# Kernel tuning notes

Measured on AMD Instinct MI355X. Metric: run time of the kernel, lower is better.

## Reference

```python
import jax, jax.numpy as jnp
import numpy as np

N_USER = 60000
N_ITEM = 40000
N = N_USER + N_ITEM          # 100000 nodes
D = 64                       # embed / layer dim
NNZ = 1600000                # edges per relation (avg degree 16)
B = 16384                    # batch of (user,item) pairs
NLAYERS = 2                  # layers=[64,64,64] -> 2 GNN layers
VAL_SCALE = 0.02             # ~1/degree, mimics symmetric-normalized Laplacian values
W_SCALE = 0.05


def spmm(row, col, val, X):
    # sparse [N,N] @ dense [N,D] via gather + segment-sum (COO)
    return jax.ops.segment_sum(val[:, None] * X[col], row, num_segments=N)


def setup_inputs() -> dict:
    key = jax.random.key(0)
    ks = jax.random.split(key, 40)
    inp = {}
    inp['userIdx'] = jax.random.randint(ks[0], (B,), 0, N_USER, dtype=jnp.int32)
    inp['itemIdx'] = jax.random.randint(ks[1], (B,), 0, N_ITEM, dtype=jnp.int32)
    inp['uEmbd'] = jax.random.normal(ks[2], (N_USER, D), dtype=jnp.float32)
    inp['iEmbd'] = jax.random.normal(ks[3], (N_ITEM, D), dtype=jnp.float32)
    for i, name in enumerate(['lap', 'trust', 'add']):
        inp[name + '_row'] = jax.random.randint(ks[4 + 3 * i], (NNZ,), 0, N, dtype=jnp.int32)
        inp[name + '_col'] = jax.random.randint(ks[5 + 3 * i], (NNZ,), 0, N, dtype=jnp.int32)
        inp[name + '_val'] = jax.random.uniform(ks[6 + 3 * i], (NNZ,), dtype=jnp.float32) * VAL_SCALE
    j = 13
    for name in ['lin_W', 'inter_W', 'attM_W', 'attA_W', 'attT_W']:
        inp[name] = jax.random.normal(ks[j], (NLAYERS, D, D), dtype=jnp.float32) * W_SCALE; j += 1
    for name in ['lin_b', 'inter_b', 'attM_b', 'attA_b', 'attT_b']:
        inp[name] = jax.random.normal(ks[j], (NLAYERS, D), dtype=jnp.float32) * W_SCALE; j += 1
    for name in ['a_main', 'a_add', 'a_trust']:
        inp[name] = jax.random.normal(ks[j], (NLAYERS, D, 1), dtype=jnp.float32) * W_SCALE; j += 1
    inp['W1'] = jax.random.normal(ks[j], (2 * D, 64), dtype=jnp.float32) * W_SCALE; j += 1
    inp['b1'] = jax.random.normal(ks[j], (64,), dtype=jnp.float32) * W_SCALE; j += 1
    inp['W2'] = jax.random.normal(ks[j], (64, 32), dtype=jnp.float32) * W_SCALE; j += 1
    inp['b2'] = jax.random.normal(ks[j], (32,), dtype=jnp.float32) * W_SCALE; j += 1
    inp['W3'] = jax.random.normal(ks[j], (32, 1), dtype=jnp.float32) * W_SCALE; j += 1
    inp['b3'] = jax.random.normal(ks[j], (1,), dtype=jnp.float32) * W_SCALE; j += 1
    return inp


def _gcf_forward(userIdx, itemIdx, uEmbd, iEmbd,
                 lap_row, lap_col, lap_val,
                 trust_row, trust_col, trust_val,
                 add_row, add_col, add_val,
                 lin_W, lin_b, inter_W, inter_b,
                 attM_W, attM_b, attA_W, attA_b, attT_W, attT_b,
                 a_main, a_add, a_trust,
                 W1, b1, W2, b2, W3, b3):
    feats = jnp.concatenate([uEmbd, iEmbd], axis=0)  # [N, D]
    all_emb = [feats]
    rels = [(lap_row, lap_col, lap_val),
            (trust_row, trust_col, trust_val),
            (add_row, add_col, add_val)]
    for l in range(NLAYERS):
        X = feats
        X2 = X * X  # inter_feature = features * features

        def relation(edges, aW, ab, avec):
            row, col, val = edges
            # (L + I) @ X  -> linear ; L @ (X*X) -> interActTransform
            h1 = (spmm(row, col, val, X) + X) @ lin_W[l] + lin_b[l]
            h2 = spmm(row, col, val, X2) @ inter_W[l] + inter_b[l]
            att = jnp.tanh((h1 + h2) @ aW + ab) @ avec  # [N, 1]
            return h1, h2, att.mean()

        m1, m2, w_main = relation(rels[0], attM_W[l], attM_b[l], a_main[l])
        t1, t2, w_trust = relation(rels[1], attT_W[l], attT_b[l], a_trust[l])
        a1, a2, w_add = relation(rels[2], attA_W[l], attA_b[l], a_add[l])
        beta = jax.nn.softmax(jnp.stack([w_main, w_add, w_trust]))  # [3]
        feats = (beta[0] * (m1 + m2) + beta[1] * (a1 + a2) + beta[2] * (t1 + t2))
        all_emb.append(feats)
    final = jnp.mean(jnp.stack(all_emb, axis=1), axis=1)  # [N, D]
    userE = final[userIdx]
    itemE = final[itemIdx + N_USER]
    h = jnp.concatenate([userE, itemE], axis=1)  # [B, 2D]
    h = jax.nn.relu(h @ W1 + b1)
    h = h @ W2 + b2
    h = h @ W3 + b3
    prediction = h.reshape(-1)
    return prediction, userE, itemE, final


def reference(userIdx, itemIdx, uEmbd, iEmbd,
              lap_row, lap_col, lap_val,
              trust_row, trust_col, trust_val,
              add_row, add_col, add_val,
              lin_W, lin_b, inter_W, inter_b,
              attM_W, attM_b, attA_W, attA_b, attT_W, attT_b,
              a_main, a_add, a_trust,
              W1, b1, W2, b2, W3, b3):
    return _gcf_forward(userIdx, itemIdx, uEmbd, iEmbd,
                        lap_row, lap_col, lap_val,
                        trust_row, trust_col, trust_val,
                        add_row, add_col, add_val,
                        lin_W, lin_b, inter_W, inter_b,
                        attM_W, attM_b, attA_W, attA_b, attT_W, attT_b,
                        a_main, a_add, a_trust,
                        W1, b1, W2, b2, W3, b3)
```

## Files before the change

### kernel.cpp

```cpp
#include <hip/hip_runtime.h>

#define N_USER  60000
#define N_ITEM  40000
#define NN      100000
#define NNZ_E   1600000
#define BB      16384
#define ND      6400000
#define ND4     1600000
#define NCHUNK  6250
#define NBUCK   196
#define BUCK_CAP 9216
#define BUCKTOT (NBUCK * BUCK_CAP)
#define BINB    196
#define EPB     8192

typedef __attribute__((ext_vector_type(8))) short bf16x8;
typedef __attribute__((ext_vector_type(8))) unsigned short u16x8;
typedef __attribute__((ext_vector_type(4))) float f32x4;

__device__ __forceinline__ float tanh_fast(float x) {
    x = fminf(fmaxf(x, -15.f), 15.f);
    float e = __expf(2.f * x);
    return (e - 1.f) / (e + 1.f);
}

__device__ __forceinline__ float bcast(float x, int k) {
    return __int_as_float(__builtin_amdgcn_readlane(__float_as_int(x), k));
}

__device__ __forceinline__ unsigned short f2bf(float f) {
    unsigned u = __float_as_uint(f);
    u += 0x7FFFu + ((u >> 16) & 1u);
    return (unsigned short)(u >> 16);
}
__device__ __forceinline__ float bf2f(unsigned short s) {
    return __uint_as_float(((unsigned)s) << 16);
}

__device__ __forceinline__ int widx(int k, int n) {
    return ((((n >> 4) * 2 + (k >> 5)) * 4 + ((k >> 3) & 3)) * 16 + (n & 15)) * 8 + (k & 7);
}

__global__ __launch_bounds__(256) void init_kernel(
    const float4* __restrict__ u, const float4* __restrict__ it,
    ushort* __restrict__ XB, float4* __restrict__ fs,
    int* __restrict__ CURS, float* __restrict__ attsum)
{
    int i = blockIdx.x * 256 + threadIdx.x;
    if (i < ND4) {
        float4 v = (i < N_USER * 16) ? u[i] : it[i - N_USER * 16];
        fs[i] = v;
        ushort4 b;
        b.x = f2bf(v.x); b.y = f2bf(v.y); b.z = f2bf(v.z); b.w = f2bf(v.w);
        ((ushort4*)XB)[i] = b;
    }
    if (i < 3 * NBUCK) CURS[i] = (i % NBUCK) * BUCK_CAP;
    if (i < 6) attsum[i] = 0.f;
}

__global__ __launch_bounds__(512) void bin_kernel(
    const int* __restrict__ rows0, const int* __restrict__ cols0, const float* __restrict__ vals0,
    const int* __restrict__ rows1, const int* __restrict__ cols1, const float* __restrict__ vals1,
    const int* __restrict__ rows2, const int* __restrict__ cols2, const float* __restrict__ vals2,
    int* __restrict__ CURS, int2* __restrict__ ECV)
{
    int rel = blockIdx.x / BINB;
    int blk = blockIdx.x % BINB;
    const int* rows; const int* cols; const float* vals;
    if (rel == 0) { rows = rows0; cols = cols0; vals = vals0; }
    else if (rel == 1) { rows = rows1; cols = cols1; vals = vals1; }
    else { rows = rows2; cols = cols2; vals = vals2; }
    long long* out = (long long*)(ECV + (size_t)rel * BUCKTOT);

    __shared__ int2 sStage[EPB];
    __shared__ int hW[8 * NBUCK];
    __shared__ int lOff[NBUCK], lEnd[NBUCK], lCur[NBUCK], gB[NBUCK];
    __shared__ int wt[4];

    int t = threadIdx.x;
    int lane = t & 63, w = t >> 6;
    for (int i = t; i < 8 * NBUCK; i += 512) hW[i] = 0;
    __syncthreads();

    int base = blk * EPB;
    int myrow[16];
    #pragma unroll
    for (int j = 0; j < 16; ++j) {
        int idx = base + j * 512 + t;
        myrow[j] = (idx < NNZ_E) ? __builtin_nontemporal_load(&rows[idx]) : -1;
        if (myrow[j] >= 0) atomicAdd(&hW[w * NBUCK + (myrow[j] >> 9)], 1);
    }
    __syncthreads();
    if (t < 256) {
        int h = 0;
        if (t < NBUCK) {
            #pragma unroll
            for (int ww = 0; ww < 8; ++ww) h += hW[ww * NBUCK + t];
        }
        int sc = h;
        #pragma unroll
        for (int o = 1; o < 64; o <<= 1) {
            int u = __shfl_up(sc, o);
            if (lane >= o) sc += u;
        }
        if (lane == 63) wt[w] = sc;
        __syncthreads();
        int woff = 0;
        #pragma unroll
        for (int ww = 0; ww < 4; ++ww) if (ww < w) woff += wt[ww];
        int excl = woff + sc - h;
        if (t < NBUCK) {
            lOff[t] = excl;
            lEnd[t] = excl + h;
            lCur[t] = excl;
            gB[t] = h ? atomicAdd(&CURS[rel * NBUCK + t], h) : 0;
        }
    } else {
        __syncthreads();
    }
    __syncthreads();
    #pragma unroll
    for (int j = 0; j < 16; ++j) {
        int idx = base + j * 512 + t;
        if (myrow[j] >= 0) {
            int c = __builtin_nontemporal_load(&cols[idx]);
            float v = __builtin_nontemporal_load(&vals[idx]);
            int b = myrow[j] >> 9;
            int pos = atomicAdd(&lCur[b], 1);
            int2 e;
            e.x = ((myrow[j] & 511) << 17) | c;
            e.y = __float_as_int(v);
            sStage[pos] = e;
        }
    }
    __syncthreads();
    for (int b = w; b < NBUCK; b += 8) {
        int s = lOff[b], e = lEnd[b];
        int gb = gB[b];
        int lim = (b + 1) * BUCK_CAP;
        for (int i = s + lane; i < e; i += 64) {
            int d = gb + (i - s);
            if (d < lim) {
                int2 ev = sStage[i];
                long long packed = (((long long)(unsigned)ev.y) << 32) | (unsigned)ev.x;
                __builtin_nontemporal_store(packed, &out[d]);
            }
        }
    }
}

__global__ __launch_bounds__(512) void bsort_kernel(
    const int* __restrict__ CURS, int2* __restrict__ ECV,
    int* __restrict__ RPS, int* __restrict__ RPE)
{
    int rel = blockIdx.x / NBUCK;
    int b   = blockIdx.x % NBUCK;
    int start = b * BUCK_CAP;
    int cnt = CURS[rel * NBUCK + b] - start;
    if (cnt > BUCK_CAP) cnt = BUCK_CAP;
    int2* ecv = ECV + (size_t)rel * BUCKTOT;

    __shared__ int2 sStage[BUCK_CAP];
    __shared__ int sOff[512], sCnt[512];
    __shared__ int wt[8];
    int t = threadIdx.x;
    int lane = t & 63, w = t >> 6;
    sCnt[t] = 0;
    __syncthreads();
    int2 e[18];
    #pragma unroll
    for (int j = 0; j < 18; ++j) {
        int i = t + j * 512;
        if (i < cnt) {
            e[j] = ecv[start + i];
            atomicAdd(&sCnt[((unsigned)e[j].x) >> 17], 1);
        }
    }
    __syncthreads();
    int h = sCnt[t];
    int sc = h;
    #pragma unroll
    for (int o = 1; o < 64; o <<= 1) {
        int u = __shfl_up(sc, o);
        if (lane >= o) sc += u;
    }
    if (lane == 63) wt[w] = sc;
    __syncthreads();
    int woff = 0;
    #pragma unroll
    for (int ww = 0; ww < 8; ++ww) if (ww < w) woff += wt[ww];
    int excl = woff + sc - h;
    __syncthreads();
    sOff[t] = excl;
    sCnt[t] = excl;
    __syncthreads();
    #pragma unroll
    for (int j = 0; j < 18; ++j) {
        int i = t + j * 512;
        if (i < cnt) {
            int rl = ((unsigned)e[j].x) >> 17;
            int pos = atomicAdd(&sCnt[rl], 1);
            int2 o2; o2.x = e[j].x & 0x1FFFF; o2.y = e[j].y;
            sStage[pos] = o2;
        }
    }
    __syncthreads();
    for (int i = t; i < cnt; i += 512) ecv[start + i] = sStage[i];
    int row = b * 512 + t;
    if (row < NN) {
        RPS[rel * NN + row] = start + sOff[t];
        RPE[rel * NN + row] = start + sCnt[t];
    }
}

__global__ __launch_bounds__(256, 4) void spmm_kernel(
    const int* __restrict__ RPS, const int* __restrict__ RPE,
    const int2* __restrict__ ecv,
    const ushort* __restrict__ XB, ushort* __restrict__ G)
{
    int t = threadIdx.x;
    int lane = t & 63;
    int wv = t >> 6;
    int dl = lane & 7;
    int r = blockIdx.x * 32 + wv * 8 + (lane >> 3);
    int ea = RPS[r], eb = RPE[r];
    int cnt = eb - ea;
    int cm = cnt;
    cm = max(cm, __shfl_xor(cm, 8));
    cm = max(cm, __shfl_xor(cm, 16));
    cm = max(cm, __shfl_xor(cm, 32));
    u16x8 xo8 = *(const u16x8*)&XB[(size_t)r * 64 + 8 * dl];
    float s1[8] = {0.f, 0.f, 0.f, 0.f, 0.f, 0.f, 0.f, 0.f};
    float s2[8] = {0.f, 0.f, 0.f, 0.f, 0.f, 0.f, 0.f, 0.f};
    for (int base = 0; base < cm; base += 4) {
        float vv[4]; u16x8 xx[4];
        #pragma unroll
        for (int j = 0; j < 4; ++j) {
            int i = base + j;
            bool ok = i < cnt;
            int is = ea + (ok ? i : 0);
            int2 cv = ecv[is];
            vv[j] = ok ? __int_as_float(cv.y) : 0.f;
            xx[j] = *(const u16x8*)&XB[(size_t)cv.x * 64 + 8 * dl];
        }
        #pragma unroll
        for (int j = 0; j < 4; ++j) {
            float v = vv[j];
            #pragma unroll
            for (int d = 0; d < 8; ++d) {
                float x = bf2f(xx[j][d]);
                s1[d] += v * x;
                s2[d] += v * x * x;
            }
        }
    }
    u16x8 o1, o2;
    #pragma unroll
    for (int d = 0; d < 8; ++d) {
        o1[d] = f2bf(s1[d] + bf2f(xo8[d]));
        o2[d] = f2bf(s2[d]);
    }
    *(u16x8*)&G[(size_t)r * 128 + 8 * dl]      = o1;
    *(u16x8*)&G[(size_t)r * 128 + 64 + 8 * dl] = o2;
}

__global__ __launch_bounds__(256) void dense_kernel(
    const ushort* __restrict__ G, ushort* __restrict__ Hout,
    const float* __restrict__ linW, const float* __restrict__ interW,
    const float* __restrict__ linb, const float* __restrict__ interb,
    const float* __restrict__ attW, const float* __restrict__ attb,
    const float* __restrict__ avec, float* __restrict__ attsum)
{
    __shared__ short sL[4096], sI[4096], sW[4096];
    __shared__ float sH[4 * 16 * 65];
    __shared__ float sBias[64], sAttb[64], sAvec[64];

    int tid = threadIdx.x;
    for (int i = tid; i < 4096; i += 256) {
        int k = i >> 6, n = i & 63, ix = widx(k, n);
        sL[ix] = (short)f2bf(linW[i]);
        sI[ix] = (short)f2bf(interW[i]);
        sW[ix] = (short)f2bf(attW[i]);
    }
    if (tid < 64) {
        sBias[tid] = linb[tid] + interb[tid];
        sAttb[tid] = attb[tid];
        sAvec[tid] = avec[tid];
    }
    __syncthreads();

    const bf16x8* pL = (const bf16x8*)sL;
    const bf16x8* pI = (const bf16x8*)sI;
    const bf16x8* pW = (const bf16x8*)sW;

    int lane = tid & 63;
    int wv = tid >> 6;
    int nl = lane & 15;
    int q  = lane >> 4;
    float* myH = sH + wv * (16 * 65);
    int gw = blockIdx.x * 4 + wv;
    int nw = gridDim.x * 4;
    float att_acc = 0.f;

    for (int c = gw; c < NCHUNK; c += nw) {
        int r0 = c * 16;
        const bf16x8* gp = (const bf16x8*)(G + (size_t)(r0 + nl) * 128);
        bf16x8 Ah[2], Qh[2];
        Ah[0] = gp[q];         Ah[1] = gp[4 + q];
        Qh[0] = gp[8 + q];     Qh[1] = gp[12 + q];
        #pragma unroll
        for (int nt = 0; nt < 4; ++nt) {
            float b = sBias[nt * 16 + nl];
            f32x4 acc = {b, b, b, b};
            #pragma unroll
            for (int kh = 0; kh < 2; ++kh) {
                int f = ((nt * 2 + kh) * 4 + q) * 16 + nl;
                acc = __builtin_amdgcn_mfma_f32_16x16x32_bf16(Ah[kh], pL[f], acc, 0, 0, 0);
                acc = __builtin_amdgcn_mfma_f32_16x16x32_bf16(Qh[kh], pI[f], acc, 0, 0, 0);
            }
            #pragma unroll
            for (int reg = 0; reg < 4; ++reg) {
                int row = q * 4 + reg;
                Hout[(size_t)(r0 + row) * 64 + nt * 16 + nl] = f2bf(acc[reg]);
                myH[row * 65 + nt * 16 + nl] = acc[reg];
            }
        }
        bf16x8 Th[2];
        #pragma unroll
        for (int kh = 0; kh < 2; ++kh) {
            #pragma unroll
            for (int j = 0; j < 8; ++j)
                Th[kh][j] = (short)f2bf(myH[nl * 65 + kh * 32 + q * 8 + j]);
        }
        #pragma unroll
        for (int nt = 0; nt < 4; ++nt) {
            float b = sAttb[nt * 16 + nl];
            f32x4 acc = {b, b, b, b};
            #pragma unroll
            for (int kh = 0; kh < 2; ++kh) {
                int f = ((nt * 2 + kh) * 4 + q) * 16 + nl;
                acc = __builtin_amdgcn_mfma_f32_16x16x32_bf16(Th[kh], pW[f], acc, 0, 0, 0);
            }
            float av = sAvec[nt * 16 + nl];
            #pragma unroll
            for (int reg = 0; reg < 4; ++reg)
                att_acc += tanh_fast(acc[reg]) * av;
        }
    }
    #pragma unroll
    for (int o = 32; o >= 1; o >>= 1) att_acc += __shfl_xor(att_acc, o);
    if (lane == 0) atomicAdd(attsum, att_acc);
}

__global__ __launch_bounds__(256) void combine_kernel(
    const ushort4* __restrict__ hM, const ushort4* __restrict__ hA,
    const ushort4* __restrict__ hT, const float* __restrict__ attsum,
    ushort4* __restrict__ XB, float4* __restrict__ fs, float scale)
{
    float w0 = attsum[0] * (1.f / NN);
    float w1 = attsum[1] * (1.f / NN);
    float w2 = attsum[2] * (1.f / NN);
    float m = fmaxf(w0, fmaxf(w1, w2));
    float e0 = __expf(w0 - m), e1 = __expf(w1 - m), e2 = __expf(w2 - m);
    float inv = 1.f / (e0 + e1 + e2);
    float b0 = e0 * inv, b1 = e1 * inv, b2 = e2 * inv;

    int i = blockIdx.x * 256 + threadIdx.x;
    if (i >= ND4) return;
    ushort4 um = hM[i], ua = hA[i], ut = hT[i];
    float4 x;
    x.x = b0 * bf2f(um.x) + b1 * bf2f(ua.x) + b2 * bf2f(ut.x);
    x.y = b0 * bf2f(um.y) + b1 * bf2f(ua.y) + b2 * bf2f(ut.y);
    x.z = b0 * bf2f(um.z) + b1 * bf2f(ua.z) + b2 * bf2f(ut.z);
    x.w = b0 * bf2f(um.w) + b1 * bf2f(ua.w) + b2 * bf2f(ut.w);
    ushort4 bo;
    bo.x = f2bf(x.x); bo.y = f2bf(x.y); bo.z = f2bf(x.z); bo.w = f2bf(x.w);
    XB[i] = bo;
    float4 f = fs[i];
    f.x = (f.x + x.x) * scale;
    f.y = (f.y + x.y) * scale;
    f.z = (f.z + x.z) * scale;
    f.w = (f.w + x.w) * scale;
    fs[i] = f;
}

__global__ __launch_bounds__(256) void mlp_kernel(
    const int* __restrict__ userIdx, const int* __restrict__ itemIdx,
    const float* __restrict__ fin,
    const float* __restrict__ W1, const float* __restrict__ b1,
    const float* __restrict__ W2, const float* __restrict__ b2,
    const float* __restrict__ W3, const float* __restrict__ b3,
    float* __restrict__ pred, float* __restrict__ userE, float* __restrict__ itemE)
{
    __shared__ float sW1[128 * 64];
    __shared__ float sW2[64 * 32];
    __shared__ float sW3[32];
    __shared__ float sb1[64];
    __shared__ float sb2[32];
    int tid = threadIdx.x;
    for (int i = tid; i < 8192; i += 256) sW1[i] = W1[i];
    for (int i = tid; i < 2048; i += 256) sW2[i] = W2[i];
    if (tid < 32) sW3[tid] = W3[tid];
    if (tid < 64) sb1[tid] = b1[tid];
    if (tid < 32) sb2[tid] = b2[tid];
    __syncthreads();
    float bb3 = b3[0];

    int lane = tid & 63;
    int gw = blockIdx.x * 4 + (tid >> 6);
    int nw = gridDim.x * 4;
    for (int p = gw; p < BB; p += nw) {
        int u = userIdx[p];
        int it = itemIdx[p] + N_USER;
        float ue = fin[u * 64 + lane];
        float ie = fin[it * 64 + lane];
        userE[p * 64 + lane] = ue;
        itemE[p * 64 + lane] = ie;
        float h = sb1[lane];
        #pragma unroll
        for (int k = 0; k < 64; ++k) h = fmaf(bcast(ue, k), sW1[k * 64 + lane], h);
        #pragma unroll
        for (int k = 0; k < 64; ++k) h = fmaf(bcast(ie, k), sW1[(k + 64) * 64 + lane], h);
        h = fmaxf(h, 0.f);
        float h2 = sb2[lane & 31];
        #pragma unroll
        for (int k = 0; k < 64; ++k) h2 = fmaf(bcast(h, k), sW2[k * 32 + (lane & 31)], h2);
        float c = (lane < 32) ? h2 * sW3[lane] : 0.f;
        #pragma unroll
        for (int o = 32; o >= 1; o >>= 1) c += __shfl_xor(c, o);
        if (lane == 0) pred[p] = c + bb3;
    }
}

extern "C" void kernel_launch(void* const* d_in, const int* in_sizes, int n_in,
                              void* d_out, int out_size, void* d_ws, size_t ws_size,
                              hipStream_t stream)
{
    const int*   userIdx = (const int*)d_in[0];
    const int*   itemIdx = (const int*)d_in[1];
    const float* uEmbd   = (const float*)d_in[2];
    const float* iEmbd   = (const float*)d_in[3];
    const int*   e_row[3] = {(const int*)d_in[4],  (const int*)d_in[10], (const int*)d_in[7]};
    const int*   e_col[3] = {(const int*)d_in[5],  (const int*)d_in[11], (const int*)d_in[8]};
    const float* e_val[3] = {(const float*)d_in[6], (const float*)d_in[12], (const float*)d_in[9]};
    const float* lin_W   = (const float*)d_in[13];
    const float* inter_W = (const float*)d_in[14];
    const float* attM_W  = (const float*)d_in[15];
    const float* attA_W  = (const float*)d_in[16];
    const float* attT_W  = (const float*)d_in[17];
    const float* lin_b   = (const float*)d_in[18];
    const float* inter_b = (const float*)d_in[19];
    const float* attM_b  = (const float*)d_in[20];
    const float* attA_b  = (const float*)d_in[21];
    const float* attT_b  = (const float*)d_in[22];
    const float* a_main  = (const float*)d_in[23];
    const float* a_add   = (const float*)d_in[24];
    const float* a_trust = (const float*)d_in[25];
    const float* W1 = (const float*)d_in[26];
    const float* b1 = (const float*)d_in[27];
    const float* W2 = (const float*)d_in[28];
    const float* b2 = (const float*)d_in[29];
    const float* W3 = (const float*)d_in[30];
    const float* b3 = (const float*)d_in[31];

    const float* attWq[3] = {attM_W, attA_W, attT_W};
    const float* attbq[3] = {attM_b, attA_b, attT_b};
    const float* avecq[3] = {a_main, a_add, a_trust};

    ushort* G  = (ushort*)d_ws;
    ushort* H0 = G + (size_t)NN * 128;
    ushort* H1 = H0 + ND;
    ushort* H2 = H1 + ND;
    int2*   ECV = (int2*)(H2 + ND);
    ushort* XB = (ushort*)(ECV + 3 * (size_t)BUCKTOT);
    int*    RPS = (int*)(XB + ND);
    int*    RPE = RPS + 3 * NN;
    int*    CURS = RPE + 3 * NN;
    float*  ATT = (float*)(CURS + 3 * NBUCK);

    ushort* Hs[3] = {H0, H1, H2};

    float* outPred  = (float*)d_out;
    float* outUser  = outPred + BB;
    float* outItem  = outUser + BB * 64;
    float* outFinal = outItem + BB * 64;

    init_kernel<<<6250, 256, 0, stream>>>((const float4*)uEmbd, (const float4*)iEmbd,
                                          XB, (float4*)outFinal, CURS, ATT);
    bin_kernel<<<3 * BINB, 512, 0, stream>>>(
        e_row[0], e_col[0], e_val[0],
        e_row[1], e_col[1], e_val[1],
        e_row[2], e_col[2], e_val[2], CURS, ECV);
    bsort_kernel<<<3 * NBUCK, 512, 0, stream>>>(CURS, ECV, RPS, RPE);

    for (int l = 0; l < 2; ++l) {
        const float* lw = lin_W + l * 4096;
        const float* iw = inter_W + l * 4096;
        const float* lb = lin_b + l * 64;
        const float* ib = inter_b + l * 64;

        for (int q = 0; q < 3; ++q) {
            spmm_kernel<<<3125, 256, 0, stream>>>(
                RPS + q * NN, RPE + q * NN, ECV + (size_t)q * BUCKTOT, XB, G);
            dense_kernel<<<512, 256, 0, stream>>>(
                G, Hs[q], lw, iw, lb, ib,
                attWq[q] + l * 4096, attbq[q] + l * 64, avecq[q] + l * 64,
                ATT + l * 3 + q);
        }
        combine_kernel<<<6250, 256, 0, stream>>>(
            (const ushort4*)Hs[0], (const ushort4*)Hs[1], (const ushort4*)Hs[2],
            ATT + l * 3, (ushort4*)XB, (float4*)outFinal,
            (l == 1) ? (1.f / 3.f) : 1.f);
    }

    mlp_kernel<<<512, 256, 0, stream>>>(userIdx, itemIdx, outFinal,
                                        W1, b1, W2, b2, W3, b3,
                                        outPred, outUser, outItem);
}
```

Measured before the change: 781.7 us.

## Precompute bf16 weights once, prefetch edge data in SpMM, widen dense grid

Adds a prep kernel that converts all layer weights to bf16 in swizzled layout once, stored in the output user buffer before it is overwritten. Dense kernels then read weights straight from global memory instead of converting them into shared memory per block, and run with four times as many blocks. A per-block reduction now replaces the per-wave attention atomics. The SpMM loop software-prefetches the next four edge records with nontemporal loads. The bin kernel uses more blocks with half the edges each. Reading weights from global instead of LDS may add latency, and reusing the output buffer as scratch relies on the MLP writing it later.

Result: slower. 838.3 us (+7.2%).

```diff
diff --git a/kernel.cpp b/kernel.cpp
--- a/kernel.cpp
+++ b/kernel.cpp
@@ -11,8 +11,8 @@
 #define NBUCK   196
 #define BUCK_CAP 9216
 #define BUCKTOT (NBUCK * BUCK_CAP)
-#define BINB    196
-#define EPB     8192
+#define BINB    391
+#define EPB     4096
 
 typedef __attribute__((ext_vector_type(8))) short bf16x8;
 typedef __attribute__((ext_vector_type(8))) unsigned short u16x8;
@@ -58,6 +58,27 @@
     if (i < 6) attsum[i] = 0.f;
 }
 
+__global__ __launch_bounds__(256) void prep_kernel(
+    const float* __restrict__ lin_W, const float* __restrict__ inter_W,
+    const float* __restrict__ attM_W, const float* __restrict__ attA_W,
+    const float* __restrict__ attT_W, ushort* __restrict__ WF)
+{
+    int b = blockIdx.x;
+    int l = b / 5, m = b % 5;
+    const float* src;
+    if (m == 0) src = lin_W;
+    else if (m == 1) src = inter_W;
+    else if (m == 2) src = attM_W;
+    else if (m == 3) src = attA_W;
+    else src = attT_W;
+    src += (size_t)l * 4096;
+    ushort* dst = WF + ((size_t)l * 5 + m) * 4096;
+    for (int i = threadIdx.x; i < 4096; i += 256) {
+        int k = i >> 6, n = i & 63;
+        dst[widx(k, n)] = f2bf(src[i]);
+    }
+}
+
 __global__ __launch_bounds__(512) void bin_kernel(
     const int* __restrict__ rows0, const int* __restrict__ cols0, const float* __restrict__ vals0,
     const int* __restrict__ rows1, const int* __restrict__ cols1, const float* __restrict__ vals1,
@@ -83,9 +104,9 @@
     __syncthreads();
 
     int base = blk * EPB;
-    int myrow[16];
-    #pragma unroll
-    for (int j = 0; j < 16; ++j) {
+    int myrow[8];
+    #pragma unroll
+    for (int j = 0; j < 8; ++j) {
         int idx = base + j * 512 + t;
         myrow[j] = (idx < NNZ_E) ? __builtin_nontemporal_load(&rows[idx]) : -1;
         if (myrow[j] >= 0) atomicAdd(&hW[w * NBUCK + (myrow[j] >> 9)], 1);
@@ -120,7 +141,7 @@
     }
     __syncthreads();
     #pragma unroll
-    for (int j = 0; j < 16; ++j) {
+    for (int j = 0; j < 8; ++j) {
         int idx = base + j * 512 + t;
         if (myrow[j] >= 0) {
             int c = __builtin_nontemporal_load(&cols[idx]);
@@ -232,16 +253,30 @@
     u16x8 xo8 = *(const u16x8*)&XB[(size_t)r * 64 + 8 * dl];
     float s1[8] = {0.f, 0.f, 0.f, 0.f, 0.f, 0.f, 0.f, 0.f};
     float s2[8] = {0.f, 0.f, 0.f, 0.f, 0.f, 0.f, 0.f, 0.f};
+
+    int cvx[4]; float cvv[4];
+    #pragma unroll
+    for (int j = 0; j < 4; ++j) {
+        int i = (j < cnt) ? j : 0;
+        long long p = __builtin_nontemporal_load((const long long*)(ecv + ea + i));
+        cvx[j] = (int)p;
+        cvv[j] = __int_as_float((int)(p >> 32));
+    }
     for (int base = 0; base < cm; base += 4) {
-        float vv[4]; u16x8 xx[4];
+        u16x8 xx[4]; float vv[4];
         #pragma unroll
         for (int j = 0; j < 4; ++j) {
-            int i = base + j;
-            bool ok = i < cnt;
-            int is = ea + (ok ? i : 0);
-            int2 cv = ecv[is];
-            vv[j] = ok ? __int_as_float(cv.y) : 0.f;
-            xx[j] = *(const u16x8*)&XB[(size_t)cv.x * 64 + 8 * dl];
+            vv[j] = (base + j < cnt) ? cvv[j] : 0.f;
+            xx[j] = *(const u16x8*)&XB[(size_t)cvx[j] * 64 + 8 * dl];
+        }
+        int nx[4]; float nv[4];
+        #pragma unroll
+        for (int j = 0; j < 4; ++j) {
+            int i = base + 4 + j;
+            i = (i < cnt) ? i : 0;
+            long long p = __builtin_nontemporal_load((const long long*)(ecv + ea + i));
+            nx[j] = (int)p;
+            nv[j] = __int_as_float((int)(p >> 32));
         }
         #pragma unroll
         for (int j = 0; j < 4; ++j) {
@@ -253,6 +288,8 @@
                 s2[d] += v * x * x;
             }
         }
+        #pragma unroll
+        for (int j = 0; j < 4; ++j) { cvx[j] = nx[j]; cvv[j] = nv[j]; }
     }
     u16x8 o1, o2;
     #pragma unroll
@@ -266,22 +303,17 @@
 
 __global__ __launch_bounds__(256) void dense_kernel(
     const ushort* __restrict__ G, ushort* __restrict__ Hout,
-    const float* __restrict__ linW, const float* __restrict__ interW,
+    const ushort* __restrict__ WL, const ushort* __restrict__ WI,
+    const ushort* __restrict__ WA,
     const float* __restrict__ linb, const float* __restrict__ interb,
-    const float* __restrict__ attW, const float* __restrict__ attb,
-    const float* __restrict__ avec, float* __restrict__ attsum)
-{
-    __shared__ short sL[4096], sI[4096], sW[4096];
+    const float* __restrict__ attb, const float* __restrict__ avec,
+    float* __restrict__ attsum)
+{
     __shared__ float sH[4 * 16 * 65];
     __shared__ float sBias[64], sAttb[64], sAvec[64];
+    __shared__ float sRed[4];
 
     int tid = threadIdx.x;
-    for (int i = tid; i < 4096; i += 256) {
-        int k = i >> 6, n = i & 63, ix = widx(k, n);
-        sL[ix] = (short)f2bf(linW[i]);
-        sI[ix] = (short)f2bf(interW[i]);
-        sW[ix] = (short)f2bf(attW[i]);
-    }
     if (tid < 64) {
         sBias[tid] = linb[tid] + interb[tid];
         sAttb[tid] = attb[tid];
@@ -289,9 +321,9 @@
     }
     __syncthreads();
 
-    const bf16x8* pL = (const bf16x8*)sL;
-    const bf16x8* pI = (const bf16x8*)sI;
-    const bf16x8* pW = (const bf16x8*)sW;
+    const bf16x8* pL = (const bf16x8*)WL;
+    const bf16x8* pI = (const bf16x8*)WI;
+    const bf16x8* pW = (const bf16x8*)WA;
 
     int lane = tid & 63;
     int wv = tid >> 6;
@@ -349,7 +381,9 @@
     }
     #pragma unroll
     for (int o = 32; o >= 1; o >>= 1) att_acc += __shfl_xor(att_acc, o);
-    if (lane == 0) atomicAdd(attsum, att_acc);
+    if (lane == 0) sRed[wv] = att_acc;
+    __syncthreads();
+    if (tid == 0) atomicAdd(attsum, sRed[0] + sRed[1] + sRed[2] + sRed[3]);
 }
 
 __global__ __launch_bounds__(256) void combine_kernel(
@@ -463,7 +497,6 @@
     const float* W3 = (const float*)d_in[30];
     const float* b3 = (const float*)d_in[31];
 
-    const float* attWq[3] = {attM_W, attA_W, attT_W};
     const float* attbq[3] = {attM_b, attA_b, attT_b};
     const float* avecq[3] = {a_main, a_add, a_trust};
 
@@ -485,8 +518,11 @@
     float* outItem  = outUser + BB * 64;
     float* outFinal = outItem + BB * 64;
 
+    ushort* WF = (ushort*)outUser;
+
     init_kernel<<<6250, 256, 0, stream>>>((const float4*)uEmbd, (const float4*)iEmbd,
                                           XB, (float4*)outFinal, CURS, ATT);
+    prep_kernel<<<10, 256, 0, stream>>>(lin_W, inter_W, attM_W, attA_W, attT_W, WF);
     bin_kernel<<<3 * BINB, 512, 0, stream>>>(
         e_row[0], e_col[0], e_val[0],
         e_row[1], e_col[1], e_val[1],
@@ -494,17 +530,17 @@
     bsort_kernel<<<3 * NBUCK, 512, 0, stream>>>(CURS, ECV, RPS, RPE);
 
     for (int l = 0; l < 2; ++l) {
-        const float* lw = lin_W + l * 4096;
-        const float* iw = inter_W + l * 4096;
         const float* lb = lin_b + l * 64;
         const float* ib = inter_b + l * 64;
+        ushort* WFl = WF + (size_t)l * 5 * 4096;
 
         for (int q = 0; q < 3; ++q) {
             spmm_kernel<<<3125, 256, 0, stream>>>(
                 RPS + q * NN, RPE + q * NN, ECV + (size_t)q * BUCKTOT, XB, G);
-            dense_kernel<<<512, 256, 0, stream>>>(
-                G, Hs[q], lw, iw, lb, ib,
-                attWq[q] + l * 4096, attbq[q] + l * 64, avecq[q] + l * 64,
+            dense_kernel<<<2048, 256, 0, stream>>>(
+                G, Hs[q],
+                WFl, WFl + 4096, WFl + (size_t)(2 + q) * 4096,
+                lb, ib, attbq[q] + l * 64, avecq[q] + l * 64,
                 ATT + l * 3 + q);
         }
         combine_kernel<<<6250, 256, 0, stream>>>(
```
